# Performance work log

Measured on AMD Instinct MI355X. Metric: run time of the kernel, lower is better.

Reference implementation:

```python
import jax, jax.numpy as jnp
import numpy as np

B, S, D = 1, 2048, 4096
H, HKV, HD = 32, 8, 128
MAX_SEQ = 4096
EPS = 1e-5


def rmsnorm(x, w, eps=EPS):
    var = jnp.mean(x * x, axis=-1, keepdims=True)
    return w * (x * jax.lax.rsqrt(var + eps))


def rotate_half_interleaved(x):
    x1 = x[..., ::2]
    x2 = x[..., 1::2]
    return jnp.stack((-x2, x1), axis=-1).reshape(x.shape)


def setup_inputs() -> dict:
    key = jax.random.key(0)
    ks = jax.random.split(key, 8)
    hidden_states = jax.random.normal(ks[0], (B, S, D), dtype=jnp.float32)
    # realistic interleaved RoPE tables: each frequency repeated twice along head_dim
    inv_freq = 1.0 / (10000.0 ** (np.arange(0, HD, 2, dtype=np.float32) / HD))
    pos = np.arange(S, dtype=np.float32)
    ang = pos[:, None] * inv_freq[None, :]            # [S, HD/2]
    ang = np.repeat(ang, 2, axis=-1)                   # [S, HD] interleaved
    cos = jnp.asarray(np.cos(ang))[None].repeat(B, axis=0)  # [B, S, HD]
    sin = jnp.asarray(np.sin(ang))[None].repeat(B, axis=0)
    scale = 1.0 / np.sqrt(D)
    return {
        "hidden_states": hidden_states,
        "cos": cos,
        "sin": sin,
        "k_cache": jnp.zeros((B, MAX_SEQ, HKV, HD), dtype=jnp.float32),
        "v_cache": jnp.zeros((B, MAX_SEQ, HKV, HD), dtype=jnp.float32),
        "Wq": jax.random.normal(ks[1], (D, H * HD), dtype=jnp.float32) * scale,
        "Wk": jax.random.normal(ks[2], (D, HKV * HD), dtype=jnp.float32) * scale,
        "Wv": jax.random.normal(ks[3], (D, HKV * HD), dtype=jnp.float32) * scale,
        "Wo": jax.random.normal(ks[4], (H * HD, D), dtype=jnp.float32) * scale,
        "rms_weight": jnp.ones((D,), dtype=jnp.float32),
        "position_ids": jnp.arange(S, dtype=jnp.int64 if jax.config.jax_enable_x64 else jnp.int32),
        "seq_len": S,
    }


def reference(hidden_states, cos, sin, k_cache, v_cache, Wq, Wk, Wv, Wo,
              rms_weight, position_ids, seq_len):
    residual = hidden_states
    h = rmsnorm(hidden_states, rms_weight)
    b, s = h.shape[:2]

    q = jnp.einsum('bsd,de->bse', h, Wq).reshape(b, s, H, HD)
    k = jnp.einsum('bsd,de->bse', h, Wk).reshape(b, s, HKV, HD)
    v = jnp.einsum('bsd,de->bse', h, Wv).reshape(b, s, HKV, HD)

    # interleaved RoPE, cos/sin broadcast over head axis (unsqueeze_dim=-2)
    c = cos[:, :, None, :]
    si = sin[:, :, None, :]
    q = q * c + rotate_half_interleaved(q) * si
    k = k * c + rotate_half_interleaved(k) * si

    # KV-cache scatter at position_ids (repeat_factor == 1 here)
    k_cache_new = k_cache.at[:, position_ids].set(k)
    v_cache_new = v_cache.at[:, position_ids].set(v)

    # prefill path (new_tok_seq_len > 1): causal SDPA with GQA over fresh K/V
    group = H // HKV
    k_full = jnp.repeat(k, group, axis=2)  # [b, s, H, HD]
    v_full = jnp.repeat(v, group, axis=2)
    qh = q.transpose(0, 2, 1, 3)           # bhqd
    kh = k_full.transpose(0, 2, 1, 3)
    vh = v_full.transpose(0, 2, 1, 3)
    scores = jnp.einsum('bhqd,bhkd->bhqk', qh, kh) / jnp.sqrt(jnp.float32(HD))
    causal = jnp.tril(jnp.ones((s, s), dtype=bool))
    scores = jnp.where(causal[None, None], scores, jnp.finfo(scores.dtype).min)
    probs = jax.nn.softmax(scores, axis=-1)
    attn = jnp.einsum('bhqk,bhkd->bhqd', probs, vh)
    attn = attn.transpose(0, 2, 1, 3).reshape(b, s, H * HD)

    out = jnp.einsum('bse,ed->bsd', attn, Wo)
    with_residual = residual + out
    return with_residual, k_cache_new, v_cache_new
```

## Files before the change

### kernel.cpp

```cpp
#include <hip/hip_runtime.h>
#include <hip/hip_bf16.h>
#include <cstdint>

#define S_LEN 2048
#define DMODEL 4096
#define NHEAD 32
#define NKV 8
#define HDIM 128
#define MAXSEQ 4096
#define NQKV 6144

typedef __bf16 bf16x8 __attribute__((ext_vector_type(8)));
typedef float f32x4 __attribute__((ext_vector_type(4)));
typedef short s16x4 __attribute__((ext_vector_type(4)));

__device__ __forceinline__ short f2bf(float f) {
  unsigned u = __builtin_bit_cast(unsigned, f);
  u += 0x7fffu + ((u >> 16) & 1u);
  return (short)(u >> 16);
}

__device__ __forceinline__ void gload_lds16(const void* g, const void* l) {
  __builtin_amdgcn_global_load_lds((const __attribute__((address_space(1))) unsigned*)g,
                                   (__attribute__((address_space(3))) unsigned*)(l), 16, 0, 0);
}

__global__ __launch_bounds__(256) void rmsnorm_kernel(const float* __restrict__ x,
                                                      const float* __restrict__ w,
                                                      short* __restrict__ out) {
  const int row = blockIdx.x, tid = threadIdx.x;
  const float4* xr = (const float4*)(x + (size_t)row * DMODEL);
  const float4* wr = (const float4*)w;
  float4 v[4];
  float ss = 0.f;
#pragma unroll
  for (int i = 0; i < 4; ++i) {
    v[i] = xr[tid + i * 256];
    ss += v[i].x * v[i].x + v[i].y * v[i].y + v[i].z * v[i].z + v[i].w * v[i].w;
  }
#pragma unroll
  for (int m = 32; m; m >>= 1) ss += __shfl_down(ss, m, 64);
  __shared__ float red[4];
  if ((tid & 63) == 0) red[tid >> 6] = ss;
  __syncthreads();
  float tot = red[0] + red[1] + red[2] + red[3];
  float sc = rsqrtf(tot * (1.f / DMODEL) + 1e-5f);
#pragma unroll
  for (int i = 0; i < 4; ++i) {
    float4 wv = wr[tid + i * 256];
    s16x4 o;
    o[0] = f2bf(v[i].x * sc * wv.x);
    o[1] = f2bf(v[i].y * sc * wv.y);
    o[2] = f2bf(v[i].z * sc * wv.z);
    o[3] = f2bf(v[i].w * sc * wv.w);
    *(s16x4*)&out[(size_t)row * DMODEL + (size_t)(tid + i * 256) * 4] = o;
  }
}

__global__ __launch_bounds__(256) void cast_transpose(const float* __restrict__ src,
                                                      short* __restrict__ dst,
                                                      int rows, int cols) {
  __shared__ float tile[32][33];
  const int c0 = blockIdx.x * 32, r0 = blockIdx.y * 32;
  const int tx = threadIdx.x, ty = threadIdx.y;
#pragma unroll
  for (int i = ty; i < 32; i += 8) tile[i][tx] = src[(size_t)(r0 + i) * cols + c0 + tx];
  __syncthreads();
#pragma unroll
  for (int i = ty; i < 32; i += 8)
    dst[(size_t)(c0 + i) * rows + r0 + tx] = f2bf(tile[tx][i]);
}

__global__ __launch_bounds__(256) void v_transpose(const float* __restrict__ QKV,
                                                   float* __restrict__ vc,
                                                   short* __restrict__ vt) {
  __shared__ float tile[32][33];
  const int d0 = blockIdx.x * 32, s0 = blockIdx.y * 32, g = blockIdx.z;
  const int tx = threadIdx.x, ty = threadIdx.y;
#pragma unroll
  for (int i = ty; i < 32; i += 8) {
    float v = QKV[(size_t)(s0 + i) * NQKV + (NHEAD + NKV) * HDIM + g * HDIM + d0 + tx];
    tile[i][tx] = v;
    vc[(size_t)(s0 + i) * (NKV * HDIM) + g * HDIM + d0 + tx] = v;
  }
  __syncthreads();
#pragma unroll
  for (int i = ty; i < 32; i += 8)
    vt[((size_t)g * HDIM + d0 + i) * S_LEN + s0 + tx] = f2bf(tile[tx][i]);
}

__global__ __launch_bounds__(256, 2) void gemm_bt(const short* __restrict__ A,
                                                  const short* __restrict__ Bt,
                                                  float* __restrict__ C,
                                                  const float* __restrict__ resid,
                                                  int M, int N, int K) {
  __shared__ __align__(16) short As[128 * 64];
  __shared__ __align__(16) short Bs[128 * 64];
  const int tid = threadIdx.x;
  const int lane = tid & 63, wave = tid >> 6;
  const int wr = wave >> 1, wc = wave & 1;
  const int lrow = lane & 15, quad = lane >> 4;
  const int m0 = blockIdx.y * 128, n0 = blockIdx.x * 128;
  f32x4 acc[4][4] = {};
  for (int k0 = 0; k0 < K; k0 += 64) {
#pragma unroll
    for (int c = 0; c < 4; ++c) {
      int idx = (wave * 4 + c) * 512 + lane * 8;
      int row = idx >> 6, kc = idx & 63;
      gload_lds16(A + (size_t)(m0 + row) * K + k0 + kc, &As[(wave * 4 + c) * 512]);
      gload_lds16(Bt + (size_t)(n0 + row) * K + k0 + kc, &Bs[(wave * 4 + c) * 512]);
    }
    __syncthreads();
#pragma unroll
    for (int kk = 0; kk < 2; ++kk) {
      bf16x8 af[4], bfr[4];
#pragma unroll
      for (int i = 0; i < 4; ++i)
        af[i] = *(const bf16x8*)&As[(wr * 64 + i * 16 + lrow) * 64 + kk * 32 + quad * 8];
#pragma unroll
      for (int j = 0; j < 4; ++j)
        bfr[j] = *(const bf16x8*)&Bs[(wc * 64 + j * 16 + lrow) * 64 + kk * 32 + quad * 8];
#pragma unroll
      for (int i = 0; i < 4; ++i)
#pragma unroll
        for (int j = 0; j < 4; ++j)
          acc[i][j] = __builtin_amdgcn_mfma_f32_16x16x32_bf16(af[i], bfr[j], acc[i][j], 0, 0, 0);
    }
    __syncthreads();
  }
#pragma unroll
  for (int i = 0; i < 4; ++i)
#pragma unroll
    for (int j = 0; j < 4; ++j) {
      int row = m0 + wr * 64 + i * 16 + quad * 4;
      int col = n0 + wc * 64 + j * 16 + lrow;
#pragma unroll
      for (int r = 0; r < 4; ++r) {
        float v = acc[i][j][r];
        size_t o = (size_t)(row + r) * N + col;
        if (resid) v += resid[o];
        C[o] = v;
      }
    }
}

__global__ __launch_bounds__(256) void rope_kernel(const float* __restrict__ QKV,
                                                   const float* __restrict__ cosb,
                                                   const float* __restrict__ sinb,
                                                   short* __restrict__ qo,
                                                   short* __restrict__ ko,
                                                   float* __restrict__ kc) {
  const int s = blockIdx.x, tid = threadIdx.x;
  const float4* r4 = (const float4*)(QKV + (size_t)s * NQKV);
  const float qscale = 0.08838834764831845f;
#pragma unroll
  for (int it = 0; it < 5; ++it) {
    int i = it * 256 + tid;
    float4 x = r4[i];
    int e = i * 4;
    int d = e & 127;
    float4 c = *(const float4*)&cosb[(size_t)s * HDIM + d];
    float4 si = *(const float4*)&sinb[(size_t)s * HDIM + d];
    float o0 = x.x * c.x - x.y * si.x;
    float o1 = x.y * c.y + x.x * si.y;
    float o2 = x.z * c.z - x.w * si.z;
    float o3 = x.w * c.w + x.z * si.w;
    if (e < NHEAD * HDIM) {
      int hh = e >> 7;
      s16x4 ov;
      ov[0] = f2bf(o0 * qscale); ov[1] = f2bf(o1 * qscale);
      ov[2] = f2bf(o2 * qscale); ov[3] = f2bf(o3 * qscale);
      *(s16x4*)&qo[((size_t)hh * S_LEN + s) * HDIM + d] = ov;
    } else {
      int ek = e - NHEAD * HDIM;
      int g = ek >> 7;
      s16x4 ov;
      ov[0] = f2bf(o0); ov[1] = f2bf(o1); ov[2] = f2bf(o2); ov[3] = f2bf(o3);
      *(s16x4*)&ko[((size_t)g * S_LEN + s) * HDIM + d] = ov;
      *(float4*)&kc[(size_t)s * (NKV * HDIM) + ek] = make_float4(o0, o1, o2, o3);
    }
  }
}

__global__ __launch_bounds__(256) void zero_tail(float* __restrict__ kc, float* __restrict__ vc) {
  size_t i = (size_t)blockIdx.x * 256 + threadIdx.x;
  const size_t tail4 = (size_t)(MAXSEQ - S_LEN) * NKV * HDIM / 4;
  float4 z = make_float4(0.f, 0.f, 0.f, 0.f);
  float4* kt = (float4*)(kc + (size_t)S_LEN * NKV * HDIM);
  float4* vt = (float4*)(vc + (size_t)S_LEN * NKV * HDIM);
  if (i < tail4) kt[i] = z;
  else if (i < 2 * tail4) vt[i - tail4] = z;
}

#define TKEY 128
__global__ __launch_bounds__(256, 1) void attn_kernel(const short* __restrict__ Q,
                                                      const short* __restrict__ Kb,
                                                      const short* __restrict__ Vt,
                                                      short* __restrict__ out) {
  extern __shared__ __align__(16) short smem[];
  short* Ks = smem;
  short* Vs = smem + 32768;
  short* Ps = smem + 65536;
  const int tid = threadIdx.x;
  const int lane = tid & 63, wave = tid >> 6;
  const int lrow = lane & 15, quad = lane >> 4;
  const int g = blockIdx.x & 7, p = blockIdx.x >> 3;
  const int h = g * 4 + wave;
  const float L2E = 1.44269504f;
  const short* Kg = Kb + (size_t)g * S_LEN * HDIM;
  const short* Vg = Vt + (size_t)g * HDIM * S_LEN;
  short* Pw = Ps + wave * 1024;

#pragma unroll 1
  for (int ph = 0; ph < 2; ++ph) {
    const int qt = ph ? (63 - p) : p;
    const int nt = (qt >> 2) + 1;

    bf16x8 qf[2][4];
#pragma unroll
    for (int i = 0; i < 2; ++i)
#pragma unroll
      for (int kf = 0; kf < 4; ++kf)
        qf[i][kf] = *(const bf16x8*)&Q[((size_t)h * S_LEN + qt * 32 + i * 16 + lrow) * HDIM + kf * 32 + quad * 8];

    f32x4 O[2][8] = {};
    float mrun[2][4], lrun[2][4];
#pragma unroll
    for (int i = 0; i < 2; ++i)
#pragma unroll
      for (int r = 0; r < 4; ++r) { mrun[i][r] = -1e30f; lrun[i][r] = 0.f; }

#pragma unroll
    for (int ii = 0; ii < 8; ++ii) {
      int s = (wave * 8 + ii) * 64 + lane;
      int r = s >> 4, gg = (s & 15) ^ (r & 15);
      gload_lds16(Kg + (size_t)r * HDIM + gg * 8, Ks + (wave * 8 + ii) * 512);
    }
#pragma unroll
    for (int ii = 0; ii < 8; ++ii) {
      int s = (wave * 8 + ii) * 64 + lane;
      int d = s >> 4, kg = (s & 15) ^ (d & 15);
      gload_lds16(Vg + (size_t)d * S_LEN + kg * 8, Vs + (wave * 8 + ii) * 512);
    }
    __syncthreads();

#pragma unroll 1
    for (int t = 0; t < nt; ++t) {
      const int bsel = t & 1;
      if (t + 1 < nt) {
        const int kb2 = (t + 1) * TKEY, o = (1 - bsel) * 16384;
#pragma unroll
        for (int ii = 0; ii < 8; ++ii) {
          int s = (wave * 8 + ii) * 64 + lane;
          int r = s >> 4, gg = (s & 15) ^ (r & 15);
          gload_lds16(Kg + (size_t)(kb2 + r) * HDIM + gg * 8, Ks + o + (wave * 8 + ii) * 512);
        }
#pragma unroll
        for (int ii = 0; ii < 8; ++ii) {
          int s = (wave * 8 + ii) * 64 + lane;
          int d = s >> 4, kg = (s & 15) ^ (d & 15);
          gload_lds16(Vg + (size_t)d * S_LEN + kb2 + kg * 8, Vs + o + (wave * 8 + ii) * 512);
        }
      }
      const short* Kc = Ks + bsel * 16384;
      const short* Vc = Vs + bsel * 16384;

      f32x4 sc[2][8] = {};
#pragma unroll
      for (int c = 0; c < 8; ++c) {
        int r = c * 16 + lrow;
#pragma unroll
        for (int kf = 0; kf < 4; ++kf) {
          int slot = r * 16 + ((kf * 4 + quad) ^ lrow);
          bf16x8 kfr = *(const bf16x8*)&Kc[slot * 8];
          sc[0][c] = __builtin_amdgcn_mfma_f32_16x16x32_bf16(qf[0][kf], kfr, sc[0][c], 0, 0, 0);
          sc[1][c] = __builtin_amdgcn_mfma_f32_16x16x32_bf16(qf[1][kf], kfr, sc[1][c], 0, 0, 0);
        }
      }

      const int kb = t * TKEY;
      const bool last = (t == nt - 1);
#pragma unroll
      for (int i = 0; i < 2; ++i) {
        if (last) {
#pragma unroll
          for (int c = 0; c < 8; ++c) {
            int key = kb + c * 16 + lrow;
#pragma unroll
            for (int r = 0; r < 4; ++r) {
              int row = qt * 32 + i * 16 + quad * 4 + r;
              if (key > row) sc[i][c][r] = -1e30f;
            }
          }
        }
        float tm[4];
#pragma unroll
        for (int r = 0; r < 4; ++r) tm[r] = sc[i][0][r];
#pragma unroll
        for (int c = 1; c < 8; ++c)
#pragma unroll
          for (int r = 0; r < 4; ++r) tm[r] = fmaxf(tm[r], sc[i][c][r]);
#pragma unroll
        for (int msk = 1; msk <= 8; msk <<= 1)
#pragma unroll
          for (int r = 0; r < 4; ++r) tm[r] = fmaxf(tm[r], __shfl_xor(tm[r], msk, 64));
#pragma unroll
        for (int r = 0; r < 4; ++r) {
          float nm = fmaxf(mrun[i][r], tm[r]);
          float alpha = exp2f((mrun[i][r] - nm) * L2E);
          mrun[i][r] = nm;
          lrun[i][r] *= alpha;
#pragma unroll
          for (int jd = 0; jd < 8; ++jd) O[i][jd][r] *= alpha;
        }
        float rs[4] = {0.f, 0.f, 0.f, 0.f};
#pragma unroll
        for (int c = 0; c < 8; ++c)
#pragma unroll
          for (int r = 0; r < 4; ++r) {
            float pv = exp2f((sc[i][c][r] - mrun[i][r]) * L2E);
            sc[i][c][r] = pv;
            rs[r] += pv;
          }
#pragma unroll
        for (int msk = 1; msk <= 8; msk <<= 1)
#pragma unroll
          for (int r = 0; r < 4; ++r) rs[r] += __shfl_xor(rs[r], msk, 64);
#pragma unroll
        for (int r = 0; r < 4; ++r) lrun[i][r] += rs[r];
      }

#pragma unroll
      for (int ks = 0; ks < 4; ++ks) {
#pragma unroll
        for (int i = 0; i < 2; ++i)
#pragma unroll
          for (int cc = 0; cc < 2; ++cc) {
            int c = ks * 2 + cc;
            int kg = cc * 2 + (lrow >> 3), off = lrow & 7;
#pragma unroll
            for (int r = 0; r < 4; ++r) {
              int q2 = i * 16 + quad * 4 + r;
              int slot = q2 * 4 + (kg ^ (q2 & 3) ^ ((q2 >> 2) & 3));
              Pw[slot * 8 + off] = f2bf(sc[i][c][r]);
            }
          }
        bf16x8 pa[2];
#pragma unroll
        for (int i = 0; i < 2; ++i) {
          int q2 = i * 16 + lrow;
          int slot = q2 * 4 + (quad ^ (q2 & 3) ^ ((q2 >> 2) & 3));
          pa[i] = *(const bf16x8*)&Pw[slot * 8];
        }
#pragma unroll
        for (int jd = 0; jd < 8; ++jd) {
          int d = jd * 16 + lrow;
          int slotv = d * 16 + ((ks * 4 + quad) ^ lrow);
          bf16x8 vb = *(const bf16x8*)&Vc[slotv * 8];
          O[0][jd] = __builtin_amdgcn_mfma_f32_16x16x32_bf16(pa[0], vb, O[0][jd], 0, 0, 0);
          O[1][jd] = __builtin_amdgcn_mfma_f32_16x16x32_bf16(pa[1], vb, O[1][jd], 0, 0, 0);
        }
      }
      __syncthreads();
    }

#pragma unroll
    for (int i = 0; i < 2; ++i)
#pragma unroll
      for (int r = 0; r < 4; ++r) {
        float inv = 1.f / lrun[i][r];
        int row = qt * 32 + i * 16 + quad * 4 + r;
#pragma unroll
        for (int jd = 0; jd < 8; ++jd)
          out[(size_t)row * DMODEL + h * HDIM + jd * 16 + lrow] = f2bf(O[i][jd][r] * inv);
      }
    __syncthreads();
  }
}

extern "C" void kernel_launch(void* const* d_in, const int* in_sizes, int n_in,
                              void* d_out, int out_size, void* d_ws, size_t ws_size,
                              hipStream_t stream) {
  const float* hs   = (const float*)d_in[0];
  const float* cosb = (const float*)d_in[1];
  const float* sinb = (const float*)d_in[2];
  const float* Wq   = (const float*)d_in[5];
  const float* Wk   = (const float*)d_in[6];
  const float* Wv   = (const float*)d_in[7];
  const float* Wo   = (const float*)d_in[8];
  const float* rmsw = (const float*)d_in[9];

  float* outp = (float*)d_out;
  float* kc = outp + (size_t)S_LEN * DMODEL;
  float* vc = kc + (size_t)MAXSEQ * NKV * HDIM;

  char* p = (char*)d_ws;
  short* h_bf  = (short*)p; p += (size_t)S_LEN * DMODEL * 2;
  short* WqkvT = (short*)p; p += (size_t)NQKV * DMODEL * 2;
  short* WoT   = (short*)p; p += (size_t)DMODEL * DMODEL * 2;
  float* QKV   = (float*)p; p += (size_t)S_LEN * NQKV * 4;
  short* q_bf  = (short*)p; p += (size_t)NHEAD * S_LEN * HDIM * 2;
  short* k_bf  = (short*)p; p += (size_t)NKV * S_LEN * HDIM * 2;
  short* vt_bf = (short*)p; p += (size_t)NKV * HDIM * S_LEN * 2;
  short* attn_bf = h_bf;

  const int ATTN_LDS = 139264;
  hipFuncSetAttribute(reinterpret_cast<const void*>(attn_kernel),
                      hipFuncAttributeMaxDynamicSharedMemorySize, ATTN_LDS);

  rmsnorm_kernel<<<S_LEN, 256, 0, stream>>>(hs, rmsw, h_bf);
  cast_transpose<<<dim3(DMODEL / 32, DMODEL / 32), dim3(32, 8), 0, stream>>>(Wq, WqkvT, DMODEL, DMODEL);
  cast_transpose<<<dim3(1024 / 32, DMODEL / 32), dim3(32, 8), 0, stream>>>(Wk, WqkvT + (size_t)DMODEL * DMODEL, DMODEL, 1024);
  cast_transpose<<<dim3(1024 / 32, DMODEL / 32), dim3(32, 8), 0, stream>>>(Wv, WqkvT + (size_t)5120 * DMODEL, DMODEL, 1024);
  cast_transpose<<<dim3(DMODEL / 32, DMODEL / 32), dim3(32, 8), 0, stream>>>(Wo, WoT, DMODEL, DMODEL);
  gemm_bt<<<dim3(NQKV / 128, S_LEN / 128), 256, 0, stream>>>(h_bf, WqkvT, QKV, nullptr, S_LEN, NQKV, DMODEL);
  rope_kernel<<<S_LEN, 256, 0, stream>>>(QKV, cosb, sinb, q_bf, k_bf, kc);
  v_transpose<<<dim3(HDIM / 32, S_LEN / 32, NKV), dim3(32, 8), 0, stream>>>(QKV, vc, vt_bf);
  zero_tail<<<4096, 256, 0, stream>>>(kc, vc);
  attn_kernel<<<256, 256, ATTN_LDS, stream>>>(q_bf, k_bf, vt_bf, attn_bf);
  gemm_bt<<<dim3(DMODEL / 128, S_LEN / 128), 256, 0, stream>>>(attn_bf, WoT, outp, hs, S_LEN, DMODEL, DMODEL);
}
```

Before: 665.0 us.

## Run both causal query tiles concurrently in attention; remap GEMM blocks per XCD

The attention kernel now uses 512 threads: four waves handle the early query tile and four the mirrored late tile. The two tiles share one staged K/V stream instead of running as two sequential phases. This halves the per-wave staging loads and reuses K/V tiles across both halves, but waves on the short tile sit idle through later iterations and LDS grows. Separately, the GEMM remaps block IDs so each XCD works on a contiguous band of N columns, aiming for better L2 reuse of B tiles.

After: 722.0 us. +8.6%, slower.

```diff
diff --git a/kernel.cpp b/kernel.cpp
--- a/kernel.cpp
+++ b/kernel.cpp
@@ -100,7 +100,16 @@
   const int lane = tid & 63, wave = tid >> 6;
   const int wr = wave >> 1, wc = wave & 1;
   const int lrow = lane & 15, quad = lane >> 4;
-  const int m0 = blockIdx.y * 128, n0 = blockIdx.x * 128;
+  int nb, mb;
+  {
+    int gx = gridDim.x, bid = blockIdx.y * gx + blockIdx.x;
+    if ((gx & 7) == 0) {
+      int xcd = bid & 7, local = bid >> 3, bandw = gx >> 3;
+      nb = xcd * bandw + local % bandw;
+      mb = local / bandw;
+    } else { nb = blockIdx.x; mb = blockIdx.y; }
+  }
+  const int m0 = mb * 128, n0 = nb * 128;
   f32x4 acc[4][4] = {};
   for (int k0 = 0; k0 < K; k0 += 64) {
 #pragma unroll
@@ -193,7 +202,7 @@
 }
 
 #define TKEY 128
-__global__ __launch_bounds__(256, 1) void attn_kernel(const short* __restrict__ Q,
+__global__ __launch_bounds__(512, 2) void attn_kernel(const short* __restrict__ Q,
                                                       const short* __restrict__ Kb,
                                                       const short* __restrict__ Vt,
                                                       short* __restrict__ out) {
@@ -205,63 +214,54 @@
   const int lane = tid & 63, wave = tid >> 6;
   const int lrow = lane & 15, quad = lane >> 4;
   const int g = blockIdx.x & 7, p = blockIdx.x >> 3;
-  const int h = g * 4 + wave;
+  const int half = wave >> 2, hw = wave & 3;
+  const int h = g * 4 + hw;
+  const int qt = half ? (63 - p) : p;
+  const int myNt = (qt >> 2) + 1;
+  const int ntMax = ((63 - p) >> 2) + 1;
   const float L2E = 1.44269504f;
   const short* Kg = Kb + (size_t)g * S_LEN * HDIM;
   const short* Vg = Vt + (size_t)g * HDIM * S_LEN;
   short* Pw = Ps + wave * 1024;
 
+  auto stage = [&](int kb2, int off) {
+#pragma unroll
+    for (int ii = 0; ii < 4; ++ii) {
+      int s = (wave * 4 + ii) * 64 + lane;
+      int r = s >> 4, gg = (s & 15) ^ (r & 15);
+      gload_lds16(Kg + (size_t)(kb2 + r) * HDIM + gg * 8, Ks + off + (wave * 4 + ii) * 512);
+    }
+#pragma unroll
+    for (int ii = 0; ii < 4; ++ii) {
+      int s = (wave * 4 + ii) * 64 + lane;
+      int d = s >> 4, kg = (s & 15) ^ (d & 15);
+      gload_lds16(Vg + (size_t)d * S_LEN + kb2 + kg * 8, Vs + off + (wave * 4 + ii) * 512);
+    }
+  };
+
+  bf16x8 qf[2][4];
+#pragma unroll
+  for (int i = 0; i < 2; ++i)
+#pragma unroll
+    for (int kf = 0; kf < 4; ++kf)
+      qf[i][kf] = *(const bf16x8*)&Q[((size_t)h * S_LEN + qt * 32 + i * 16 + lrow) * HDIM + kf * 32 + quad * 8];
+
+  f32x4 O[2][8] = {};
+  float mrun[2][4], lrun[2][4];
+#pragma unroll
+  for (int i = 0; i < 2; ++i)
+#pragma unroll
+    for (int r = 0; r < 4; ++r) { mrun[i][r] = -1e30f; lrun[i][r] = 0.f; }
+
+  stage(0, 0);
+  __syncthreads();
+
 #pragma unroll 1
-  for (int ph = 0; ph < 2; ++ph) {
-    const int qt = ph ? (63 - p) : p;
-    const int nt = (qt >> 2) + 1;
-
-    bf16x8 qf[2][4];
-#pragma unroll
-    for (int i = 0; i < 2; ++i)
-#pragma unroll
-      for (int kf = 0; kf < 4; ++kf)
-        qf[i][kf] = *(const bf16x8*)&Q[((size_t)h * S_LEN + qt * 32 + i * 16 + lrow) * HDIM + kf * 32 + quad * 8];
-
-    f32x4 O[2][8] = {};
-    float mrun[2][4], lrun[2][4];
-#pragma unroll
-    for (int i = 0; i < 2; ++i)
-#pragma unroll
-      for (int r = 0; r < 4; ++r) { mrun[i][r] = -1e30f; lrun[i][r] = 0.f; }
-
-#pragma unroll
-    for (int ii = 0; ii < 8; ++ii) {
-      int s = (wave * 8 + ii) * 64 + lane;
-      int r = s >> 4, gg = (s & 15) ^ (r & 15);
-      gload_lds16(Kg + (size_t)r * HDIM + gg * 8, Ks + (wave * 8 + ii) * 512);
-    }
-#pragma unroll
-    for (int ii = 0; ii < 8; ++ii) {
-      int s = (wave * 8 + ii) * 64 + lane;
-      int d = s >> 4, kg = (s & 15) ^ (d & 15);
-      gload_lds16(Vg + (size_t)d * S_LEN + kg * 8, Vs + (wave * 8 + ii) * 512);
-    }
-    __syncthreads();
-
-#pragma unroll 1
-    for (int t = 0; t < nt; ++t) {
-      const int bsel = t & 1;
-      if (t + 1 < nt) {
-        const int kb2 = (t + 1) * TKEY, o = (1 - bsel) * 16384;
-#pragma unroll
-        for (int ii = 0; ii < 8; ++ii) {
-          int s = (wave * 8 + ii) * 64 + lane;
-          int r = s >> 4, gg = (s & 15) ^ (r & 15);
-          gload_lds16(Kg + (size_t)(kb2 + r) * HDIM + gg * 8, Ks + o + (wave * 8 + ii) * 512);
-        }
-#pragma unroll
-        for (int ii = 0; ii < 8; ++ii) {
-          int s = (wave * 8 + ii) * 64 + lane;
-          int d = s >> 4, kg = (s & 15) ^ (d & 15);
-          gload_lds16(Vg + (size_t)d * S_LEN + kb2 + kg * 8, Vs + o + (wave * 8 + ii) * 512);
-        }
-      }
+  for (int t = 0; t < ntMax; ++t) {
+    const int bsel = t & 1;
+    if (t + 1 < ntMax) stage((t + 1) * TKEY, (1 - bsel) * 16384);
+
+    if (t < myNt) {
       const short* Kc = Ks + bsel * 16384;
       const short* Vc = Vs + bsel * 16384;
 
@@ -279,7 +279,7 @@
       }
 
       const int kb = t * TKEY;
-      const bool last = (t == nt - 1);
+      const bool last = (t == myNt - 1);
 #pragma unroll
       for (int i = 0; i < 2; ++i) {
         if (last) {
@@ -361,21 +361,20 @@
           O[1][jd] = __builtin_amdgcn_mfma_f32_16x16x32_bf16(pa[1], vb, O[1][jd], 0, 0, 0);
         }
       }
-      __syncthreads();
-    }
-
-#pragma unroll
-    for (int i = 0; i < 2; ++i)
-#pragma unroll
-      for (int r = 0; r < 4; ++r) {
-        float inv = 1.f / lrun[i][r];
-        int row = qt * 32 + i * 16 + quad * 4 + r;
-#pragma unroll
-        for (int jd = 0; jd < 8; ++jd)
-          out[(size_t)row * DMODEL + h * HDIM + jd * 16 + lrow] = f2bf(O[i][jd][r] * inv);
-      }
+    }
     __syncthreads();
   }
+
+#pragma unroll
+  for (int i = 0; i < 2; ++i)
+#pragma unroll
+    for (int r = 0; r < 4; ++r) {
+      float inv = 1.f / lrun[i][r];
+      int row = qt * 32 + i * 16 + quad * 4 + r;
+#pragma unroll
+      for (int jd = 0; jd < 8; ++jd)
+        out[(size_t)row * DMODEL + h * HDIM + jd * 16 + lrow] = f2bf(O[i][jd][r] * inv);
+    }
 }
 
 extern "C" void kernel_launch(void* const* d_in, const int* in_sizes, int n_in,
@@ -404,7 +403,7 @@
   short* vt_bf = (short*)p; p += (size_t)NKV * HDIM * S_LEN * 2;
   short* attn_bf = h_bf;
 
-  const int ATTN_LDS = 139264;
+  const int ATTN_LDS = 147456;
   hipFuncSetAttribute(reinterpret_cast<const void*>(attn_kernel),
                       hipFuncAttributeMaxDynamicSharedMemorySize, ATTN_LDS);
 
@@ -417,6 +416,6 @@
   rope_kernel<<<S_LEN, 256, 0, stream>>>(QKV, cosb, sinb, q_bf, k_bf, kc);
   v_transpose<<<dim3(HDIM / 32, S_LEN / 32, NKV), dim3(32, 8), 0, stream>>>(QKV, vc, vt_bf);
   zero_tail<<<4096, 256, 0, stream>>>(kc, vc);
-  attn_kernel<<<256, 256, ATTN_LDS, stream>>>(q_bf, k_bf, vt_bf, attn_bf);
+  attn_kernel<<<256, 512, ATTN_LDS, stream>>>(q_bf, k_bf, vt_bf, attn_bf);
   gemm_bt<<<dim3(DMODEL / 128, S_LEN / 128), 256, 0, stream>>>(attn_bf, WoT, outp, hs, S_LEN, DMODEL, DMODEL);
 }
```
